# Optimization experiments

Hardware: AMD Instinct MI355X
Metric: run time of the kernel (lower is better)

The kernel has to match this reference:

```python
import jax, jax.numpy as jnp
import numpy as np
from jax import lax
from jax.scipy.special import logsumexp

N = 1024   # keypoints image 0
M = 1024   # keypoints image 1
D = 256    # descriptor dim
H = 4      # attention heads
L = 18     # GNN layers ('self','cross')*9
ITERS = 100
KENC = [4, 32, 64, 128, 256]


def conv1(x, w, b):
    # 1x1 Conv1d == channel matmul: x [b,c,n], w [o,c], b [o]
    return jnp.einsum('oc,bcn->bon', w, x) + b[None, :, None]


def inorm(x, eps=1e-5):
    # InstanceNorm1d (affine=False): normalize over length per (b, c)
    m = jnp.mean(x, axis=-1, keepdims=True)
    v = jnp.var(x, axis=-1, keepdims=True)
    return (x - m) * lax.rsqrt(v + eps)


def attention_block(x, src, pw, pb, mw, mb):
    b, d, _ = x.shape
    dh = d // H
    q = conv1(x, pw[0], pb[0]).reshape(b, dh, H, -1)
    k = conv1(src, pw[1], pb[1]).reshape(b, dh, H, -1)
    v = conv1(src, pw[2], pb[2]).reshape(b, dh, H, -1)
    s = jnp.einsum('bdhn,bdhm->bhnm', q, k) / (dh ** 0.5)
    p = jax.nn.softmax(s, axis=-1)
    o = jnp.einsum('bhnm,bdhm->bdhn', p, v).reshape(b, d, -1)
    return conv1(o, mw, mb)


def prop(x, src, i, Pw, Pb, Mw, Mb, W0, B0, W1, B1):
    msg = attention_block(x, src, Pw[i], Pb[i], Mw[i], Mb[i])
    h = jnp.concatenate([x, msg], axis=1)          # [b, 2D, n]
    h = jax.nn.relu(inorm(conv1(h, W0[i], B0[i])))
    return conv1(h, W1[i], B1[i])


def sinkhorn(Z, log_mu, log_nu, iters):
    def step(carry, _):
        u, v = carry
        u = log_mu - logsumexp(Z + v[:, None, :], axis=2)
        v = log_nu - logsumexp(Z + u[:, :, None], axis=1)
        return (u, v), None
    init = (jnp.zeros_like(log_mu), jnp.zeros_like(log_nu))
    (u, v), _ = lax.scan(jax.checkpoint(step), init, None, length=iters)
    return Z + u[:, :, None] + v[:, None, :]


def log_optimal_transport(scores, alpha, iters):
    b, m, n = scores.shape
    bins0 = jnp.broadcast_to(alpha, (b, m, 1))
    bins1 = jnp.broadcast_to(alpha, (b, 1, n))
    binsA = jnp.broadcast_to(alpha, (b, 1, 1))
    couplings = jnp.concatenate([
        jnp.concatenate([scores, bins0], axis=-1),
        jnp.concatenate([bins1, binsA], axis=-1)], axis=1)  # [b, m+1, n+1]
    norm = np.float32(-np.log(m + n))
    log_mu = jnp.concatenate([jnp.full((m,), norm, scores.dtype),
                              jnp.array([np.log(n)], scores.dtype) + norm])
    log_nu = jnp.concatenate([jnp.full((n,), norm, scores.dtype),
                              jnp.array([np.log(m)], scores.dtype) + norm])
    log_mu = jnp.broadcast_to(log_mu[None], (b, m + 1))
    log_nu = jnp.broadcast_to(log_nu[None], (b, n + 1))
    Z = sinkhorn(couplings, log_mu, log_nu, iters)
    return Z - norm


def setup_inputs() -> dict:
    key = jax.random.key(0)
    ks = iter(jax.random.split(key, 64))
    w = lambda shape, s=0.02: jax.random.normal(next(ks), shape, jnp.float32) * s
    inp = {
        'keypoints0': jax.random.normal(next(ks), (1, N, 3), jnp.float32),
        'keypoints1': jax.random.normal(next(ks), (1, M, 3), jnp.float32),
        'descriptors0': jax.random.normal(next(ks), (1, D, N), jnp.float32),
        'descriptors1': jax.random.normal(next(ks), (1, D, M), jnp.float32),
        'scores0': jax.random.uniform(next(ks), (1, N), jnp.float32),
        'scores1': jax.random.uniform(next(ks), (1, M), jnp.float32),
    }
    for i in range(4):
        inp[f'kenc_w{i}'] = w((KENC[i + 1], KENC[i]), 0.1)
        inp[f'kenc_b{i}'] = jnp.zeros((KENC[i + 1],), jnp.float32)
    inp['gnn_proj_w'] = w((L, 3, D, D))
    inp['gnn_proj_b'] = jnp.zeros((L, 3, D), jnp.float32)
    inp['gnn_merge_w'] = w((L, D, D))
    inp['gnn_merge_b'] = jnp.zeros((L, D), jnp.float32)
    inp['gnn_mlp_w0'] = w((L, 2 * D, 2 * D))
    inp['gnn_mlp_b0'] = jnp.zeros((L, 2 * D), jnp.float32)
    inp['gnn_mlp_w1'] = w((L, D, 2 * D))
    inp['gnn_mlp_b1'] = jnp.zeros((L, D), jnp.float32)
    inp['final_w'] = w((D, D))
    inp['final_b'] = jnp.zeros((D,), jnp.float32)
    inp['bin_score'] = jnp.float32(1.0)
    return inp


def reference(keypoints0, keypoints1, descriptors0, descriptors1, scores0, scores1,
              kenc_w0, kenc_b0, kenc_w1, kenc_b1, kenc_w2, kenc_b2, kenc_w3, kenc_b3,
              gnn_proj_w, gnn_proj_b, gnn_merge_w, gnn_merge_b,
              gnn_mlp_w0, gnn_mlp_b0, gnn_mlp_w1, gnn_mlp_b1,
              final_w, final_b, bin_score):
    def kenc(kpts, sc):
        h = jnp.concatenate([jnp.swapaxes(kpts, 1, 2), sc[:, None, :]], axis=1)  # [b,4,n]
        h = jax.nn.relu(inorm(conv1(h, kenc_w0, kenc_b0)))
        h = jax.nn.relu(inorm(conv1(h, kenc_w1, kenc_b1)))
        h = jax.nn.relu(inorm(conv1(h, kenc_w2, kenc_b2)))
        return conv1(h, kenc_w3, kenc_b3)

    d0 = descriptors0 + kenc(keypoints0, scores0)
    d1 = descriptors1 + kenc(keypoints1, scores1)
    for i in range(L):  # even: self, odd: cross
        cross = (i % 2 == 1)
        s0 = d1 if cross else d0
        s1 = d0 if cross else d1
        delta0 = prop(d0, s0, i, gnn_proj_w, gnn_proj_b, gnn_merge_w, gnn_merge_b,
                      gnn_mlp_w0, gnn_mlp_b0, gnn_mlp_w1, gnn_mlp_b1)
        delta1 = prop(d1, s1, i, gnn_proj_w, gnn_proj_b, gnn_merge_w, gnn_merge_b,
                      gnn_mlp_w0, gnn_mlp_b0, gnn_mlp_w1, gnn_mlp_b1)
        d0, d1 = d0 + delta0, d1 + delta1
    md0 = conv1(d0, final_w, final_b)
    md1 = conv1(d1, final_w, final_b)
    scores = jnp.einsum('bdn,bdm->bnm', md0, md1) / (D ** 0.5)
    return log_optimal_transport(scores, bin_score, ITERS)
```

## Files before the change

### kernel.cpp

```cpp
#include <hip/hip_runtime.h>
#include <cstddef>

#define TPB 256

typedef _Float16 f16;
typedef _Float16 f16x4 __attribute__((ext_vector_type(4)));
typedef _Float16 f16x8 __attribute__((ext_vector_type(8)));
typedef float f32x4 __attribute__((ext_vector_type(4)));
typedef unsigned long long u64;

__device__ __forceinline__ float block_sum(float v, float* red) {
  int tid = threadIdx.x;
  red[tid] = v; __syncthreads();
#pragma unroll
  for (int off = 128; off > 0; off >>= 1) {
    if (tid < off) red[tid] += red[tid + off];
    __syncthreads();
  }
  float r = red[0];
  __syncthreads();
  return r;
}

__global__ __launch_bounds__(TPB) void build_h0(const float* __restrict__ kp0,
                                                const float* __restrict__ kp1,
                                                const float* __restrict__ sc0,
                                                const float* __restrict__ sc1,
                                                float* __restrict__ h0) {
  int n = blockIdx.x * TPB + threadIdx.x;
  int im = blockIdx.y;
  const float* kp = im ? kp1 : kp0;
  const float* sc = im ? sc1 : sc0;
  float* h = h0 + (size_t)im * 4096;
  h[n]        = kp[n * 3 + 0];
  h[1024 + n] = kp[n * 3 + 1];
  h[2048 + n] = kp[n * 3 + 2];
  h[3072 + n] = sc[n];
}

template<bool NORMRELU, bool RESID>
__global__ __launch_bounds__(TPB) void chanconv(const float* __restrict__ W,
                                                const float* __restrict__ bias,
                                                const float* __restrict__ in, long instride,
                                                const float* res0, const float* res1,
                                                float* __restrict__ out, long outstride, int C) {
  int o = blockIdx.x, im = blockIdx.y, tid = threadIdx.x;
  const float* inp = in + (long)im * instride;
  __shared__ float Ws[128];
  __shared__ float red[TPB];
  for (int c = tid; c < C; c += TPB) Ws[c] = W[(long)o * C + c];
  __syncthreads();
  float b = bias[o];
  float4 acc = {b, b, b, b};
  for (int c = 0; c < C; ++c) {
    float w = Ws[c];
    float4 v = *(const float4*)(inp + (long)c * 1024 + tid * 4);
    acc.x += w * v.x; acc.y += w * v.y; acc.z += w * v.z; acc.w += w * v.w;
  }
  float* orow = out + (long)im * outstride + (long)o * 1024;
  if (NORMRELU) {
    float s = acc.x + acc.y + acc.z + acc.w;
    float mean = block_sum(s, red) * (1.f / 1024.f);
    float dx = acc.x - mean, dy = acc.y - mean, dz = acc.z - mean, dw = acc.w - mean;
    float var = block_sum(dx * dx + dy * dy + dz * dz + dw * dw, red) * (1.f / 1024.f);
    float rstd = rsqrtf(var + 1e-5f);
    float4 o4 = {fmaxf(dx * rstd, 0.f), fmaxf(dy * rstd, 0.f),
                 fmaxf(dz * rstd, 0.f), fmaxf(dw * rstd, 0.f)};
    *(float4*)(orow + tid * 4) = o4;
  } else {
    if (RESID) {
      const float* res = im ? res1 : res0;
      float4 r = *(const float4*)(res + (long)o * 1024 + tid * 4);
      acc.x += r.x; acc.y += r.y; acc.z += r.z; acc.w += r.w;
    }
    *(float4*)(orow + tid * 4) = acc;
  }
}

struct GBH {
  const void* A; const void* B; const void* B2; void* C;
  const float* bias; const float* res; const float* mu; const float* rs;
  void* o2a; void* o2b; int coff; int pad;
};
struct GB16 { GBH g[16]; };

#define F_BNORM   1
#define F_BCONCAT 2
#define F_BADD    4
#define F_CD16    8
#define F_RES     16
#define F_OUT2    32
#define F_CSCAT   64

template<int BM, int BN, int ASRC, int BSRC, int FLAGS>
__global__ __launch_bounds__(TPB) void gemmh(GB16 gbs, int K, int lda, int ldb,
                                             int ldc, float alpha, int ksplit) {
  constexpr int WM = BM / 32;
  constexpr int NWN = 4 / WM;
  constexpr int WN = BN / NWN;
  constexpr int NFR = WN / 16;
  GBH g = gbs.g[blockIdx.z];
  const int tid = threadIdx.x;
  const int lane = tid & 63, wid = tid >> 6;
  const int wm = wid / NWN, wn = wid % NWN;
  const int m0 = blockIdx.y * BM, n0 = blockIdx.x * BN;
  __shared__ f16 As[BM][36];
  __shared__ f16 Bs[BN][36];
  f32x4 acc[2][NFR];
#pragma unroll
  for (int i = 0; i < 2; ++i)
#pragma unroll
    for (int j = 0; j < NFR; ++j) acc[i][j] = (f32x4){0.f, 0.f, 0.f, 0.f};

  for (int k0 = 0; k0 < K; k0 += 32) {
    if constexpr (ASRC == 0) {
      if constexpr (BM == 64) {
        const int m = tid >> 2, k4 = (tid & 3) * 8;
        const float* ap = (const float*)g.A + (long)(m0 + m) * lda + k0 + k4;
        float4 u0 = *(const float4*)ap, u1 = *(const float4*)(ap + 4);
        f16x4 h0 = {(f16)u0.x, (f16)u0.y, (f16)u0.z, (f16)u0.w};
        f16x4 h1 = {(f16)u1.x, (f16)u1.y, (f16)u1.z, (f16)u1.w};
        *(f16x4*)&As[m][k4] = h0;
        *(f16x4*)&As[m][k4 + 4] = h1;
      } else {
        const int m = tid >> 3, k4 = (tid & 7) * 4;
        const float* ap = (const float*)g.A + (long)(m0 + m) * lda + k0 + k4;
        float4 u0 = *(const float4*)ap;
        f16x4 h0 = {(f16)u0.x, (f16)u0.y, (f16)u0.z, (f16)u0.w};
        *(f16x4*)&As[m][k4] = h0;
      }
    } else if constexpr (ASRC == 1) {
      const int k = tid >> 3, mg = (tid & 7) * 8;
      const f16* ap = (const f16*)g.A + (long)(k0 + k) * lda + m0 + mg;
      f16x8 h = *(const f16x8*)ap;
#pragma unroll
      for (int j = 0; j < 8; ++j) As[mg + j][k] = h[j];
    } else {
      const int m = tid >> 2, k4 = (tid & 3) * 8;
      const f16* ap = (const f16*)g.A + (long)(m0 + m) * lda + k0 + k4;
      f16x8 h = *(const f16x8*)ap;
      const float M = g.mu[m0 + m], Iv = g.rs[m0 + m];
      f16x4 h0, h1;
#pragma unroll
      for (int j = 0; j < 4; ++j) h0[j] = (f16)(__expf((float)h[j] - M) * Iv);
#pragma unroll
      for (int j = 0; j < 4; ++j) h1[j] = (f16)(__expf((float)h[j + 4] - M) * Iv);
      *(f16x4*)&As[m][k4] = h0;
      *(f16x4*)&As[m][k4 + 4] = h1;
    }
#pragma unroll
    for (int r = 0; r < BN / 64; ++r) {
      if constexpr (BSRC == 0) {
        const int k = tid >> 3, ng = (tid & 7) * 8 + r * 64;
        const int kg = k0 + k;
        const float* bp;
        if constexpr ((FLAGS & F_BCONCAT) != 0)
          bp = (kg < ksplit) ? ((const float*)g.B + (long)kg * ldb)
                             : ((const float*)g.B2 + (long)(kg - ksplit) * ldb);
        else
          bp = (const float*)g.B + (long)kg * ldb;
        float4 u0 = *(const float4*)(bp + n0 + ng);
        float4 u1 = *(const float4*)(bp + n0 + ng + 4);
        Bs[ng + 0][k] = (f16)u0.x; Bs[ng + 1][k] = (f16)u0.y;
        Bs[ng + 2][k] = (f16)u0.z; Bs[ng + 3][k] = (f16)u0.w;
        Bs[ng + 4][k] = (f16)u1.x; Bs[ng + 5][k] = (f16)u1.y;
        Bs[ng + 6][k] = (f16)u1.z; Bs[ng + 7][k] = (f16)u1.w;
      } else if constexpr (BSRC == 1) {
        const int k = tid >> 3, ng = (tid & 7) * 8 + r * 64;
        const int kg = k0 + k;
        f16x8 h = *(const f16x8*)((const f16*)g.B + (long)kg * ldb + n0 + ng);
        if constexpr ((FLAGS & F_BNORM) != 0) {
          const float mu = g.mu[kg], rs = g.rs[kg];
#pragma unroll
          for (int j = 0; j < 8; ++j)
            h[j] = (f16)fmaxf(((float)h[j] - mu) * rs, 0.f);
        }
#pragma unroll
        for (int j = 0; j < 8; ++j) Bs[ng + j][k] = h[j];
      } else {
        const int n = (tid >> 2) + r * 64, k4 = (tid & 3) * 8;
        const f16* bp = (const f16*)g.B + (long)(n0 + n) * ldb + k0 + k4;
        f16x8 h = *(const f16x8*)bp;
        if constexpr ((FLAGS & F_BADD) != 0) {
          f16x8 h2 = *(const f16x8*)((const f16*)g.B2 + (long)(n0 + n) * ldb + k0 + k4);
          h = h + h2;
        }
        f16x4 h0 = {h[0], h[1], h[2], h[3]};
        f16x4 h1 = {h[4], h[5], h[6], h[7]};
        *(f16x4*)&Bs[n][k4] = h0;
        *(f16x4*)&Bs[n][k4 + 4] = h1;
      }
    }
    __syncthreads();
#pragma unroll
    for (int ks = 0; ks < 2; ++ks) {
      const int kof = ks * 16 + ((lane >> 4) << 2);
      f16x4 a[2], b[NFR];
      a[0] = *(const f16x4*)&As[wm * 32 + (lane & 15)][kof];
      a[1] = *(const f16x4*)&As[wm * 32 + 16 + (lane & 15)][kof];
#pragma unroll
      for (int fn = 0; fn < NFR; ++fn)
        b[fn] = *(const f16x4*)&Bs[wn * WN + fn * 16 + (lane & 15)][kof];
#pragma unroll
      for (int fm = 0; fm < 2; ++fm)
#pragma unroll
        for (int fn = 0; fn < NFR; ++fn)
          acc[fm][fn] = __builtin_amdgcn_mfma_f32_16x16x16f16(a[fm], b[fn], acc[fm][fn], 0, 0, 0);
    }
    __syncthreads();
  }

  const int r0 = (lane >> 4) << 2, cn = lane & 15;
#pragma unroll
  for (int fm = 0; fm < 2; ++fm) {
#pragma unroll
    for (int r = 0; r < 4; ++r) {
      const int m = m0 + wm * 32 + fm * 16 + r0 + r;
      const float bi = g.bias ? g.bias[m] : 0.f;
#pragma unroll
      for (int fn = 0; fn < NFR; ++fn) {
        const int n = n0 + wn * WN + fn * 16 + cn;
        float v = acc[fm][fn][r] * alpha + bi;
        if constexpr ((FLAGS & F_RES) != 0) v += g.res[(long)m * ldc + n];
        if constexpr ((FLAGS & F_OUT2) != 0) {
          ((float*)g.C)[(long)m * 1028 + n] = v;
          ((f16*)g.o2a)[(long)m * 1028 + n] = (f16)v;
          ((f16*)g.o2b)[(long)n * 1028 + m] = (f16)v;
        } else if constexpr ((FLAGS & F_CSCAT) != 0) {
          ((f16*)g.C)[(long)m * ldc + g.coff + 4 * n] = (f16)v;
        } else if constexpr ((FLAGS & F_CD16) != 0) {
          ((f16*)g.C)[(long)m * ldc + n] = (f16)v;
        } else {
          ((float*)g.C)[(long)m * ldc + n] = v;
        }
      }
    }
  }
}

__global__ __launch_bounds__(TPB) void rowlse_h(const f16* __restrict__ S,
                                                float* __restrict__ Mrow,
                                                float* __restrict__ Inv) {
  int row = blockIdx.x * 4 + (threadIdx.x >> 6);
  int lane = threadIdx.x & 63;
  const f16x8* p = (const f16x8*)(S + (long)row * 1024);
  f16x8 v0 = p[lane], v1 = p[lane + 64];
  float m = -1e30f;
#pragma unroll
  for (int j = 0; j < 8; ++j)
    m = fmaxf(m, fmaxf((float)v0[j], (float)v1[j]));
#pragma unroll
  for (int off = 32; off > 0; off >>= 1) m = fmaxf(m, __shfl_xor(m, off));
  float s = 0.f;
#pragma unroll
  for (int j = 0; j < 8; ++j)
    s += __expf((float)v0[j] - m) + __expf((float)v1[j] - m);
#pragma unroll
  for (int off = 32; off > 0; off >>= 1) s += __shfl_xor(s, off);
  if (lane == 0) { Mrow[row] = m; Inv[row] = 1.f / s; }
}

__global__ __launch_bounds__(TPB) void rowstats2_h(const f16* __restrict__ t,
                                                   float* __restrict__ mu,
                                                   float* __restrict__ rs) {
  int row = blockIdx.x * 4 + (threadIdx.x >> 6);
  int lane = threadIdx.x & 63;
  const f16x8* p = (const f16x8*)(t + (long)row * 1024);
  f16x8 v0 = p[lane], v1 = p[lane + 64];
  float s = 0.f, s2 = 0.f;
#pragma unroll
  for (int j = 0; j < 8; ++j) {
    float a = (float)v0[j], b = (float)v1[j];
    s += a + b; s2 += a * a + b * b;
  }
#pragma unroll
  for (int off = 32; off > 0; off >>= 1) { s += __shfl_xor(s, off); s2 += __shfl_xor(s2, off); }
  if (lane == 0) {
    float mean = s * (1.f / 1024.f);
    mu[row] = mean;
    rs[row] = rsqrtf(fmaxf(s2 * (1.f / 1024.f) - mean * mean, 0.f) + 1e-5f);
  }
}

#define NORMC  (-7.62461899f)
#define LOGN   (6.93147181f)
#define LOG_MN (7.62461899f)
#define ZLD    1028
#define SINKB  64

__device__ __forceinline__ u64 llc_load64(const u64* p) {
  return __hip_atomic_load(p, __ATOMIC_RELAXED, __HIP_MEMORY_SCOPE_AGENT);
}
__device__ __forceinline__ void slot_store(u64* p, float v, unsigned gen) {
  union { float f; unsigned u; } c; c.f = v;
  u64 x = ((u64)gen << 32) | (u64)c.u;
  __hip_atomic_store(p, x, __ATOMIC_RELAXED, __HIP_MEMORY_SCOPE_AGENT);
}
__device__ __forceinline__ float slot_val(u64 x) {
  union { unsigned u; float f; } c; c.u = (unsigned)x;
  return c.f;
}

__global__ __launch_bounds__(TPB) void fill_bins(float* __restrict__ Z,
                                                 const float* __restrict__ alpha_p,
                                                 u64* __restrict__ uS,
                                                 u64* __restrict__ vS) {
  float a = *alpha_p;
  int t = blockIdx.x * TPB + threadIdx.x;
  if (t <= 1024) {
    Z[(long)t * ZLD + 1024] = a;
    Z[(long)1024 * ZLD + t] = a;
    slot_store(uS + t, 0.f, 0u);
    slot_store(vS + t, 0.f, 0u);
  }
}

__device__ __forceinline__ void sink_half(const f16x8 zreg[4][2],
                                          const u64* __restrict__ w,
                                          u64* __restrict__ out,
                                          unsigned rgen, int tid, int gw, int lane,
                                          float alpha, float* __restrict__ lds) {
  __syncthreads();
#pragma unroll
  for (int q = 0; q < 4; ++q) {
    const int s = tid + q * TPB;
    u64 x;
    do { x = llc_load64(w + s); } while ((unsigned)(x >> 32) != rgen);
    lds[s] = slot_val(x);
  }
  if (tid == 0) {
    u64 x;
    do { x = llc_load64(w + 1024); } while ((unsigned)(x >> 32) != rgen);
    lds[1024] = slot_val(x);
  }
  __syncthreads();

  float vv[16];
#pragma unroll
  for (int t = 0; t < 16; ++t) vv[t] = lds[lane + 64 * t];
  const float w1024 = lds[1024];
  const float binv = alpha + w1024;
  const unsigned wgen = rgen + 1;

  float res[4];
#pragma unroll
  for (int r = 0; r < 4; ++r) {
    float val[16];
    float m = binv;
#pragma unroll
    for (int t = 0; t < 16; ++t) {
      val[t] = (float)zreg[r][t >> 3][t & 7] + vv[t];
      m = fmaxf(m, val[t]);
    }
#pragma unroll
    for (int off = 32; off > 0; off >>= 1) m = fmaxf(m, __shfl_xor(m, off));
    float s = 0.f;
#pragma unroll
    for (int t = 0; t < 16; ++t) s += __expf(val[t] - m);
#pragma unroll
    for (int off = 32; off > 0; off >>= 1) s += __shfl_xor(s, off);
    s += __expf(binv - m);
    res[r] = NORMC - (m + logf(s));
  }
  float myv = (lane == 0) ? res[0] : (lane == 1) ? res[1]
            : (lane == 2) ? res[2] : res[3];
  if (lane < 4) slot_store(out + 4 * gw + lane, myv, wgen);

  if (gw == 0) {
    float m = w1024;
#pragma unroll
    for (int t = 0; t < 16; ++t) m = fmaxf(m, vv[t]);
#pragma unroll
    for (int off = 32; off > 0; off >>= 1) m = fmaxf(m, __shfl_xor(m, off));
    float s = 0.f;
#pragma unroll
    for (int t = 0; t < 16; ++t) s += __expf(vv[t] - m);
#pragma unroll
    for (int off = 32; off > 0; off >>= 1) s += __shfl_xor(s, off);
    s += __expf(w1024 - m);
    if (lane == 0)
      slot_store(out + 1024, NORMC + LOGN - (alpha + m + logf(s)), wgen);
  }
}

__global__ __launch_bounds__(TPB) void sink_persist(const f16* __restrict__ Zh,
                                                    const f16* __restrict__ Zth,
                                                    u64* __restrict__ uS,
                                                    u64* __restrict__ vS,
                                                    const float* __restrict__ alpha_p) {
  __shared__ float lds[ZLD];
  const int tid = threadIdx.x;
  const int lane = tid & 63;
  const int gw = blockIdx.x * 4 + (tid >> 6);
  const float alpha = *alpha_p;

  f16x8 zr[4][2], zt[4][2];
#pragma unroll
  for (int r = 0; r < 4; ++r) {
    const long row = 4 * gw + r;
    const f16* zp = Zh + row * ZLD;
    const f16* ztp = Zth + row * ZLD;
#pragma unroll
    for (int hh = 0; hh < 2; ++hh)
#pragma unroll
      for (int j = 0; j < 8; ++j) {
        zr[r][hh][j] = zp[lane + 64 * (8 * hh + j)];
        zt[r][hh][j] = ztp[lane + 64 * (8 * hh + j)];
      }
  }

  unsigned gen = 0;
#pragma unroll 1
  for (int it = 0; it < 100; ++it) {
    sink_half(zr, vS, uS, gen, tid, gw, lane, alpha, lds);  ++gen;
    sink_half(zt, uS, vS, gen, tid, gw, lane, alpha, lds);  ++gen;
  }
}

__global__ __launch_bounds__(TPB) void assemble(const float* __restrict__ Z,
                                                const u64* __restrict__ uS,
                                                const u64* __restrict__ vS,
                                                float* __restrict__ out) {
  int idx = blockIdx.x * TPB + threadIdx.x;
  if (idx < 1025 * 1025) {
    int i = idx / 1025;
    int j = idx - i * 1025;
    out[idx] = Z[(long)i * ZLD + j] + slot_val(uS[i]) + slot_val(vS[j]) + LOG_MN;
  }
}

static inline GBH mkgb(const void* A, const void* B, void* C,
                       const float* bias = nullptr, const void* B2 = nullptr,
                       const float* res = nullptr,
                       const float* mu = nullptr, const float* rs = nullptr,
                       int coff = 0, void* o2a = nullptr, void* o2b = nullptr) {
  GBH g; g.A = A; g.B = B; g.B2 = B2; g.C = C; g.bias = bias; g.res = res;
  g.mu = mu; g.rs = rs; g.o2a = o2a; g.o2b = o2b; g.coff = coff; g.pad = 0;
  return g;
}

extern "C" void kernel_launch(void* const* d_in, const int* in_sizes, int n_in,
                              void* d_out, int out_size, void* d_ws, size_t ws_size,
                              hipStream_t stream) {
  const float* kp0     = (const float*)d_in[0];
  const float* kp1     = (const float*)d_in[1];
  const float* desc0   = (const float*)d_in[2];
  const float* desc1   = (const float*)d_in[3];
  const float* sc0     = (const float*)d_in[4];
  const float* sc1     = (const float*)d_in[5];
  const float* kw[4]   = {(const float*)d_in[6], (const float*)d_in[8],
                          (const float*)d_in[10], (const float*)d_in[12]};
  const float* kb[4]   = {(const float*)d_in[7], (const float*)d_in[9],
                          (const float*)d_in[11], (const float*)d_in[13]};
  const float* proj_w  = (const float*)d_in[14];
  const float* proj_b  = (const float*)d_in[15];
  const float* merge_w = (const float*)d_in[16];
  const float* merge_b = (const float*)d_in[17];
  const float* mlp_w0  = (const float*)d_in[18];
  const float* mlp_b0  = (const float*)d_in[19];
  const float* mlp_w1  = (const float*)d_in[20];
  const float* mlp_b1  = (const float*)d_in[21];
  const float* final_w = (const float*)d_in[22];
  const float* final_b = (const float*)d_in[23];
  const float* alpha_p = (const float*)d_in[24];

  float* p = (float*)d_ws;
  float* dA  = p; p += 524288;
  float* dB  = p; p += 524288;
  float* h0  = p; p += 8192;
  float* hb1 = p; p += 262144;
  float* hb2 = p; p += 131072;
  float* msg = p; p += 524288;
  float* muA = p; p += 1024;
  float* rsA = p; p += 1024;
  float* Mrw = p; p += 8192;
  float* Inv = p; p += 8192;
  float* Zb  = p; p += 1053700;
  u64* uS = (u64*)p; p += 2056;
  u64* vS = (u64*)p; p += 2056;
  f16* qkvh = (f16*)p; p += 786432;
  f16* Sh   = (f16*)p; p += 4194304;
  f16* oAh  = (f16*)p; p += 262144;
  f16* oBh  = (f16*)p; p += 262144;
  f16* tbh  = (f16*)p; p += 524288;
  f16* mdbh = (f16*)p; p += 262144;
  f16* Zh   = (f16*)p; p += 526852;
  f16* Zth  = (f16*)p; p += 526852;
  size_t need_bytes = (size_t)(p - (float*)d_ws) * sizeof(float);
  if (ws_size < need_bytes) return;

  const long DSTR = 262144;

  build_h0<<<dim3(4, 2), TPB, 0, stream>>>(kp0, kp1, sc0, sc1, h0);
  chanconv<true, false><<<dim3(32, 2),  TPB, 0, stream>>>(kw[0], kb[0], h0,  4096,   nullptr, nullptr, hb1, 32768,  4);
  chanconv<true, false><<<dim3(64, 2),  TPB, 0, stream>>>(kw[1], kb[1], hb1, 32768,  nullptr, nullptr, hb2, 65536,  32);
  chanconv<true, false><<<dim3(128, 2), TPB, 0, stream>>>(kw[2], kb[2], hb2, 65536,  nullptr, nullptr, hb1, 131072, 64);
  chanconv<false, true><<<dim3(256, 2), TPB, 0, stream>>>(kw[3], kb[3], hb1, 131072, desc0,   desc1,   dA,  DSTR,   128);

  float* dc = dA;
  float* dn = dB;
  for (int i = 0; i < 18; ++i) {
    bool cross = (i & 1) != 0;
    const float* xs[2] = {dc, dc + DSTR};
    const float* ss2[2] = {cross ? xs[1] : xs[0], cross ? xs[0] : xs[1]};

    {
      GB16 gb{};
      for (int im = 0; im < 2; ++im)
        for (int pp = 0; pp < 3; ++pp)
          gb.g[im * 3 + pp] = mkgb(proj_w + (size_t)(i * 3 + pp) * 65536,
                                   (pp == 0 ? xs[im] : ss2[im]),
                                   qkvh + (size_t)(im * 3 + pp) * DSTR,
                                   proj_b + (size_t)(i * 3 + pp) * 256);
      gemmh<32, 128, 0, 0, F_CD16><<<dim3(8, 8, 6), TPB, 0, stream>>>(
          gb, 256, 256, 1024, 1024, 1.f, 0);
    }
    {
      GB16 gb{};
      for (int im = 0; im < 2; ++im)
        for (int h = 0; h < 4; ++h)
          gb.g[im * 4 + h] = mkgb(qkvh + (size_t)(im * 3 + 0) * DSTR + h * 1024,
                                  qkvh + (size_t)(im * 3 + 1) * DSTR + h * 1024,
                                  Sh + (size_t)(im * 4 + h) * 1048576);
      gemmh<64, 128, 1, 1, F_CD16><<<dim3(8, 16, 8), TPB, 0, stream>>>(
          gb, 64, 4096, 4096, 1024, 0.125f, 0);
    }
    rowlse_h<<<2048, TPB, 0, stream>>>(Sh, Mrw, Inv);
    {
      GB16 gb{};
      for (int kh = 0; kh < 2; ++kh)
        for (int imh = 0; imh < 8; ++imh) {
          int im = imh >> 2, h = imh & 3;
          gb.g[kh * 8 + imh] = mkgb(Sh + (size_t)imh * 1048576 + kh * 512,
                                    qkvh + (size_t)(im * 3 + 2) * DSTR + h * 1024 + kh * 512,
                                    (kh ? oBh : oAh) + (size_t)im * 262144,
                                    nullptr, nullptr, nullptr,
                                    Mrw + imh * 1024, Inv + imh * 1024, h);
        }
      gemmh<64, 64, 2, 2, F_CD16 | F_CSCAT><<<dim3(1, 16, 16), TPB, 0, stream>>>(
          gb, 512, 1024, 4096, 256, 1.f, 0);
    }
    {
      GB16 gb{};
      for (int im = 0; im < 2; ++im)
        gb.g[im] = mkgb(merge_w + (size_t)i * 65536, oAh + (size_t)im * 262144,
                        msg + (size_t)im * DSTR, merge_b + (size_t)i * 256,
                        oBh + (size_t)im * 262144);
      gemmh<32, 64, 0, 2, F_BADD><<<dim3(16, 8, 2), TPB, 0, stream>>>(
          gb, 256, 256, 256, 1024, 1.f, 0);
    }
    {
      GB16 gb{};
      for (int im = 0; im < 2; ++im)
        gb.g[im] = mkgb(mlp_w0 + (size_t)i * 262144, xs[im],
                        tbh + (size_t)im * 524288, mlp_b0 + (size_t)i * 512,
                        msg + (size_t)im * DSTR);
      gemmh<64, 64, 0, 0, F_BCONCAT | F_CD16><<<dim3(16, 8, 2), TPB, 0, stream>>>(
          gb, 512, 512, 1024, 1024, 1.f, 256);
    }
    rowstats2_h<<<256, TPB, 0, stream>>>(tbh, muA, rsA);
    {
      GB16 gb{};
      for (int im = 0; im < 2; ++im)
        gb.g[im] = mkgb(mlp_w1 + (size_t)i * 131072, tbh + (size_t)im * 524288,
                        dn + (size_t)im * DSTR, mlp_b1 + (size_t)i * 256,
                        nullptr, xs[im],
                        muA + (size_t)im * 512, rsA + (size_t)im * 512);
      gemmh<32, 64, 0, 1, F_BNORM | F_RES><<<dim3(16, 8, 2), TPB, 0, stream>>>(
          gb, 512, 512, 1024, 1024, 1.f, 0);
    }
    float* tmp = dc; dc = dn; dn = tmp;
  }

  {
    GB16 gb{};
    for (int im = 0; im < 2; ++im)
      gb.g[im] = mkgb(final_w, dc + (size_t)im * DSTR, mdbh + (size_t)im * 262144,
                      final_b);
    gemmh<32, 64, 0, 0, F_CD16><<<dim3(16, 8, 2), TPB, 0, stream>>>(
        gb, 256, 256, 1024, 1024, 1.f, 0);
  }
  {
    GB16 gb{};
    gb.g[0] = mkgb(mdbh, mdbh + 262144, Zb, nullptr, nullptr, nullptr,
                   nullptr, nullptr, 0, Zh, Zth);
    gemmh<64, 64, 1, 1, F_OUT2><<<dim3(16, 16, 1), TPB, 0, stream>>>(
        gb, 256, 1024, 1024, ZLD, 0.0625f, 0);
  }
  fill_bins<<<5, TPB, 0, stream>>>(Zb, alpha_p, uS, vS);

  sink_persist<<<SINKB, TPB, 0, stream>>>(Zh, Zth, uS, vS, alpha_p);

  assemble<<<4105, TPB, 0, stream>>>(Zb, uS, vS, (float*)d_out);
}
```

Before: 2.277 ms.

## Fold merge projection into MLP first layer and fuse instance-norm stats

Each layer's merge conv is algebraically folded into the first MLP layer. A per-layer weight product W0[:,256:]·merge_w and a folded bias are precomputed once at startup, so the merge GEMM and the fp32 msg buffer go away. The MLP GEMM now reads the attention output halves directly as its second K segment. Instance-norm sums are accumulated with atomics in the MLP GEMM epilogue, which removes the rowstats kernel; the next GEMM derives mean and rstd from these sums, at the cost of atomics and a less precise E[x²]−mean² variance.

```diff
diff --git a/kernel.cpp b/kernel.cpp
--- a/kernel.cpp
+++ b/kernel.cpp
@@ -82,7 +82,7 @@
   const float* bias; const float* res; const float* mu; const float* rs;
   void* o2a; void* o2b; int coff; int pad;
 };
-struct GB16 { GBH g[16]; };
+struct GBN { GBH g[18]; };
 
 #define F_BNORM   1
 #define F_BCONCAT 2
@@ -91,9 +91,13 @@
 #define F_RES     16
 #define F_OUT2    32
 #define F_CSCAT   64
+#define F_BNORM2  128
+#define F_ACONCAT 256
+#define F_BMIX    512
+#define F_STATS   1024
 
 template<int BM, int BN, int ASRC, int BSRC, int FLAGS>
-__global__ __launch_bounds__(TPB) void gemmh(GB16 gbs, int K, int lda, int ldb,
+__global__ __launch_bounds__(TPB) void gemmh(GBN gbs, int K, int lda, int ldb,
                                              int ldc, float alpha, int ksplit) {
   constexpr int WM = BM / 32;
   constexpr int NWN = 4 / WM;
@@ -116,7 +120,15 @@
     if constexpr (ASRC == 0) {
       if constexpr (BM == 64) {
         const int m = tid >> 2, k4 = (tid & 3) * 8;
-        const float* ap = (const float*)g.A + (long)(m0 + m) * lda + k0 + k4;
+        const float* ap;
+        if constexpr ((FLAGS & F_ACONCAT) != 0) {
+          if (k0 >= ksplit)
+            ap = (const float*)g.o2a + (long)(m0 + m) * 256 + (k0 - ksplit) + k4;
+          else
+            ap = (const float*)g.A + (long)(m0 + m) * lda + k0 + k4;
+        } else {
+          ap = (const float*)g.A + (long)(m0 + m) * lda + k0 + k4;
+        }
         float4 u0 = *(const float4*)ap, u1 = *(const float4*)(ap + 4);
         f16x4 h0 = {(f16)u0.x, (f16)u0.y, (f16)u0.z, (f16)u0.w};
         f16x4 h1 = {(f16)u1.x, (f16)u1.y, (f16)u1.z, (f16)u1.w};
@@ -151,29 +163,49 @@
 #pragma unroll
     for (int r = 0; r < BN / 64; ++r) {
       if constexpr (BSRC == 0) {
-        const int k = tid >> 3, ng = (tid & 7) * 8 + r * 64;
-        const int kg = k0 + k;
-        const float* bp;
-        if constexpr ((FLAGS & F_BCONCAT) != 0)
-          bp = (kg < ksplit) ? ((const float*)g.B + (long)kg * ldb)
-                             : ((const float*)g.B2 + (long)(kg - ksplit) * ldb);
-        else
-          bp = (const float*)g.B + (long)kg * ldb;
-        float4 u0 = *(const float4*)(bp + n0 + ng);
-        float4 u1 = *(const float4*)(bp + n0 + ng + 4);
-        Bs[ng + 0][k] = (f16)u0.x; Bs[ng + 1][k] = (f16)u0.y;
-        Bs[ng + 2][k] = (f16)u0.z; Bs[ng + 3][k] = (f16)u0.w;
-        Bs[ng + 4][k] = (f16)u1.x; Bs[ng + 5][k] = (f16)u1.y;
-        Bs[ng + 6][k] = (f16)u1.z; Bs[ng + 7][k] = (f16)u1.w;
+        bool f16path = false;
+        if constexpr ((FLAGS & F_BMIX) != 0) f16path = (k0 >= ksplit);
+        if (f16path) {
+          const int n = (tid >> 2) + r * 64, k4b = (tid & 3) * 8;
+          const long off = (long)(n0 + n) * 256 + (k0 - ksplit) + k4b;
+          f16x8 h = *(const f16x8*)((const f16*)g.B2 + off)
+                  + *(const f16x8*)((const f16*)g.o2b + off);
+          f16x4 h0 = {h[0], h[1], h[2], h[3]};
+          f16x4 h1 = {h[4], h[5], h[6], h[7]};
+          *(f16x4*)&Bs[n][k4b] = h0;
+          *(f16x4*)&Bs[n][k4b + 4] = h1;
+        } else {
+          const int k = tid >> 3, ng = (tid & 7) * 8 + r * 64;
+          const int kg = k0 + k;
+          const float* bp;
+          if constexpr ((FLAGS & F_BCONCAT) != 0)
+            bp = (kg < ksplit) ? ((const float*)g.B + (long)kg * ldb)
+                               : ((const float*)g.B2 + (long)(kg - ksplit) * ldb);
+          else
+            bp = (const float*)g.B + (long)kg * ldb;
+          float4 u0 = *(const float4*)(bp + n0 + ng);
+          float4 u1 = *(const float4*)(bp + n0 + ng + 4);
+          Bs[ng + 0][k] = (f16)u0.x; Bs[ng + 1][k] = (f16)u0.y;
+          Bs[ng + 2][k] = (f16)u0.z; Bs[ng + 3][k] = (f16)u0.w;
+          Bs[ng + 4][k] = (f16)u1.x; Bs[ng + 5][k] = (f16)u1.y;
+          Bs[ng + 6][k] = (f16)u1.z; Bs[ng + 7][k] = (f16)u1.w;
+        }
       } else if constexpr (BSRC == 1) {
         const int k = tid >> 3, ng = (tid & 7) * 8 + r * 64;
         const int kg = k0 + k;
         f16x8 h = *(const f16x8*)((const f16*)g.B + (long)kg * ldb + n0 + ng);
-        if constexpr ((FLAGS & F_BNORM) != 0) {
-          const float mu = g.mu[kg], rs = g.rs[kg];
+        if constexpr ((FLAGS & (F_BNORM | F_BNORM2)) != 0) {
+          float mean, rstd;
+          if constexpr ((FLAGS & F_BNORM2) != 0) {
+            float s1 = g.mu[kg], s2 = g.rs[kg];
+            mean = s1 * (1.f / 1024.f);
+            rstd = rsqrtf(fmaxf(s2 * (1.f / 1024.f) - mean * mean, 0.f) + 1e-5f);
+          } else {
+            mean = g.mu[kg]; rstd = g.rs[kg];
+          }
 #pragma unroll
           for (int j = 0; j < 8; ++j)
-            h[j] = (f16)fmaxf(((float)h[j] - mu) * rs, 0.f);
+            h[j] = (f16)fmaxf(((float)h[j] - mean) * rstd, 0.f);
         }
 #pragma unroll
         for (int j = 0; j < 8; ++j) Bs[ng + j][k] = h[j];
@@ -217,6 +249,7 @@
     for (int r = 0; r < 4; ++r) {
       const int m = m0 + wm * 32 + fm * 16 + r0 + r;
       const float bi = g.bias ? g.bias[m] : 0.f;
+      float s1 = 0.f, s2 = 0.f;
 #pragma unroll
       for (int fn = 0; fn < NFR; ++fn) {
         const int n = n0 + wn * WN + fn * 16 + cn;
@@ -233,6 +266,18 @@
         } else {
           ((float*)g.C)[(long)m * ldc + n] = v;
         }
+        if constexpr ((FLAGS & F_STATS) != 0) { s1 += v; s2 += v * v; }
+      }
+      if constexpr ((FLAGS & F_STATS) != 0) {
+#pragma unroll
+        for (int off = 1; off < 16; off <<= 1) {
+          s1 += __shfl_xor(s1, off);
+          s2 += __shfl_xor(s2, off);
+        }
+        if ((lane & 15) == 0) {
+          atomicAdd((float*)g.mu + m, s1);
+          atomicAdd((float*)g.rs + m, s2);
+        }
       }
     }
   }
@@ -260,26 +305,22 @@
   if (lane == 0) { Mrow[row] = m; Inv[row] = 1.f / s; }
 }
 
-__global__ __launch_bounds__(TPB) void rowstats2_h(const f16* __restrict__ t,
-                                                   float* __restrict__ mu,
-                                                   float* __restrict__ rs) {
-  int row = blockIdx.x * 4 + (threadIdx.x >> 6);
-  int lane = threadIdx.x & 63;
-  const f16x8* p = (const f16x8*)(t + (long)row * 1024);
-  f16x8 v0 = p[lane], v1 = p[lane + 64];
-  float s = 0.f, s2 = 0.f;
-#pragma unroll
-  for (int j = 0; j < 8; ++j) {
-    float a = (float)v0[j], b = (float)v1[j];
-    s += a + b; s2 += a * a + b * b;
-  }
-#pragma unroll
-  for (int off = 32; off > 0; off >>= 1) { s += __shfl_xor(s, off); s2 += __shfl_xor(s2, off); }
-  if (lane == 0) {
-    float mean = s * (1.f / 1024.f);
-    mu[row] = mean;
-    rs[row] = rsqrtf(fmaxf(s2 * (1.f / 1024.f) - mean * mean, 0.f) + 1e-5f);
-  }
+__global__ __launch_bounds__(TPB) void zero_buf(float* __restrict__ p, int n) {
+  int i = blockIdx.x * TPB + threadIdx.x;
+  if (i < n) p[i] = 0.f;
+}
+
+__global__ __launch_bounds__(TPB) void bf_prep(const float* __restrict__ mlp_w0,
+                                               const float* __restrict__ mlp_b0,
+                                               const float* __restrict__ merge_b,
+                                               float* __restrict__ bfB) {
+  int idx = blockIdx.x * TPB + threadIdx.x;
+  int l = idx >> 9, m = idx & 511;
+  const float* wrow = mlp_w0 + (size_t)l * 262144 + (size_t)m * 512 + 256;
+  const float* mb = merge_b + (size_t)l * 256;
+  float s = mlp_b0[(size_t)l * 512 + m];
+  for (int j = 0; j < 256; ++j) s += wrow[j] * mb[j];
+  bfB[idx] = s;
 }
 
 #define NORMC  (-7.62461899f)
@@ -470,12 +511,13 @@
   float* h0  = p; p += 8192;
   float* hb1 = p; p += 262144;
   float* hb2 = p; p += 131072;
-  float* msg = p; p += 524288;
-  float* muA = p; p += 1024;
-  float* rsA = p; p += 1024;
   float* Mrw = p; p += 8192;
   float* Inv = p; p += 8192;
   float* Zb  = p; p += 1053700;
+  float* WfB = p; p += 2359296;
+  float* bfB = p; p += 9216;
+  float* SS1 = p; p += 18432;
+  float* SS2 = p; p += 18432;
   u64* uS = (u64*)p; p += 2056;
   u64* vS = (u64*)p; p += 2056;
   f16* qkvh = (f16*)p; p += 786432;
@@ -491,6 +533,17 @@
 
   const long DSTR = 262144;
 
+  zero_buf<<<144, TPB, 0, stream>>>(SS1, 36864);
+  {
+    GBN gb{};
+    for (int l = 0; l < 18; ++l)
+      gb.g[l] = mkgb(mlp_w0 + (size_t)l * 262144 + 256, merge_w + (size_t)l * 65536,
+                     WfB + (size_t)l * 131072);
+    gemmh<64, 64, 0, 0, 0><<<dim3(4, 8, 18), TPB, 0, stream>>>(
+        gb, 256, 512, 256, 256, 1.f, 0);
+  }
+  bf_prep<<<36, TPB, 0, stream>>>(mlp_w0, mlp_b0, merge_b, bfB);
+
   build_h0<<<dim3(4, 2), TPB, 0, stream>>>(kp0, kp1, sc0, sc1, h0);
   chanconv<true, false><<<dim3(32, 2),  TPB, 0, stream>>>(kw[0], kb[0], h0,  4096,   nullptr, nullptr, hb1, 32768,  4);
   chanconv<true, false><<<dim3(64, 2),  TPB, 0, stream>>>(kw[1], kb[1], hb1, 32768,  nullptr, nullptr, hb2, 65536,  32);
@@ -505,7 +558,7 @@
     const float* ss2[2] = {cross ? xs[1] : xs[0], cross ? xs[0] : xs[1]};
 
     {
-      GB16 gb{};
+      GBN gb{};
       for (int im = 0; im < 2; ++im)
         for (int pp = 0; pp < 3; ++pp)
           gb.g[im * 3 + pp] = mkgb(proj_w + (size_t)(i * 3 + pp) * 65536,
@@ -516,7 +569,7 @@
           gb, 256, 256, 1024, 1024, 1.f, 0);
     }
     {
-      GB16 gb{};
+      GBN gb{};
       for (int im = 0; im < 2; ++im)
         for (int h = 0; h < 4; ++h)
           gb.g[im * 4 + h] = mkgb(qkvh + (size_t)(im * 3 + 0) * DSTR + h * 1024,
@@ -527,7 +580,7 @@
     }
     rowlse_h<<<2048, TPB, 0, stream>>>(Sh, Mrw, Inv);
     {
-      GB16 gb{};
+      GBN gb{};
       for (int kh = 0; kh < 2; ++kh)
         for (int imh = 0; imh < 8; ++imh) {
           int im = imh >> 2, h = imh & 3;
@@ -541,39 +594,34 @@
           gb, 512, 1024, 4096, 256, 1.f, 0);
     }
     {
-      GB16 gb{};
-      for (int im = 0; im < 2; ++im)
-        gb.g[im] = mkgb(merge_w + (size_t)i * 65536, oAh + (size_t)im * 262144,
-                        msg + (size_t)im * DSTR, merge_b + (size_t)i * 256,
-                        oBh + (size_t)im * 262144);
-      gemmh<32, 64, 0, 2, F_BADD><<<dim3(16, 8, 2), TPB, 0, stream>>>(
-          gb, 256, 256, 256, 1024, 1.f, 0);
-    }
-    {
-      GB16 gb{};
+      GBN gb{};
       for (int im = 0; im < 2; ++im)
         gb.g[im] = mkgb(mlp_w0 + (size_t)i * 262144, xs[im],
-                        tbh + (size_t)im * 524288, mlp_b0 + (size_t)i * 512,
-                        msg + (size_t)im * DSTR);
-      gemmh<64, 64, 0, 0, F_BCONCAT | F_CD16><<<dim3(16, 8, 2), TPB, 0, stream>>>(
+                        tbh + (size_t)im * 524288, bfB + (size_t)i * 512,
+                        oAh + (size_t)im * 262144, nullptr,
+                        SS1 + (size_t)i * 1024 + im * 512,
+                        SS2 + (size_t)i * 1024 + im * 512,
+                        0, WfB + (size_t)i * 131072, oBh + (size_t)im * 262144);
+      gemmh<64, 64, 0, 0, F_CD16 | F_ACONCAT | F_BMIX | F_STATS>
+          <<<dim3(16, 8, 2), TPB, 0, stream>>>(
           gb, 512, 512, 1024, 1024, 1.f, 256);
     }
-    rowstats2_h<<<256, TPB, 0, stream>>>(tbh, muA, rsA);
     {
-      GB16 gb{};
+      GBN gb{};
       for (int im = 0; im < 2; ++im)
         gb.g[im] = mkgb(mlp_w1 + (size_t)i * 131072, tbh + (size_t)im * 524288,
                         dn + (size_t)im * DSTR, mlp_b1 + (size_t)i * 256,
                         nullptr, xs[im],
-                        muA + (size_t)im * 512, rsA + (size_t)im * 512);
-      gemmh<32, 64, 0, 1, F_BNORM | F_RES><<<dim3(16, 8, 2), TPB, 0, stream>>>(
+                        SS1 + (size_t)i * 1024 + im * 512,
+                        SS2 + (size_t)i * 1024 + im * 512);
+      gemmh<32, 64, 0, 1, F_BNORM2 | F_RES><<<dim3(16, 8, 2), TPB, 0, stream>>>(
           gb, 512, 512, 1024, 1024, 1.f, 0);
     }
     float* tmp = dc; dc = dn; dn = tmp;
   }
 
   {
-    GB16 gb{};
+    GBN gb{};
     for (int im = 0; im < 2; ++im)
       gb.g[im] = mkgb(final_w, dc + (size_t)im * DSTR, mdbh + (size_t)im * 262144,
                       final_b);
@@ -581,7 +629,7 @@
         gb, 256, 256, 1024, 1024, 1.f, 0);
   }
   {
-    GB16 gb{};
+    GBN gb{};
     gb.g[0] = mkgb(mdbh, mdbh + 262144, Zb, nullptr, nullptr, nullptr,
                    nullptr, nullptr, 0, Zh, Zth);
     gemmh<64, 64, 1, 1, F_OUT2><<<dim3(16, 16, 1), TPB, 0, stream>>>(
```

Result: no change. 2.264 ms (-0.6%).
